# Kernel optimization log

Hardware: AMD Instinct MI355X
Metric: run time of the kernel (lower is better)

## Reference

```python
import jax, jax.numpy as jnp
import numpy as np

STALENESS_LAMBDA = 0.001
TEMPERATURE = 1.0
TOP_K = 3
EPS = 1e-8


def setup_inputs() -> dict:
    key = jax.random.key(0)
    ks = jax.random.split(key, 6)
    B, D, H, E = 131072, 512, 256, 10
    features = jax.random.normal(ks[0], (B, D), dtype=jnp.float32)
    W_proj = jax.random.normal(ks[1], (D, H), dtype=jnp.float32) * 0.02
    b_proj = jnp.zeros((H,), dtype=jnp.float32)
    expert_emb = jax.random.normal(ks[2], (E, H), dtype=jnp.float32) * 0.01
    expert_features = jax.random.normal(ks[3], (E, D), dtype=jnp.float32)
    trust = jax.random.uniform(ks[4], (E,), dtype=jnp.float32)
    delta_t = jax.random.uniform(ks[5], (E,), dtype=jnp.float32) * 100.0
    return {"features": features, "W_proj": W_proj, "b_proj": b_proj,
            "expert_emb": expert_emb, "expert_features": expert_features,
            "trust": trust, "delta_t": delta_t}


def reference(features, W_proj, b_proj, expert_emb, expert_features, trust, delta_t):
    H = W_proj.shape[1]
    # learned gate: sigmoid(proj(x) . e_j / sqrt(H))  -> (B, E)
    proj = features @ W_proj + b_proj                                  # (B, H)
    gate = jax.nn.sigmoid(jnp.einsum('bh,eh->be', proj, expert_emb)
                          / jnp.sqrt(jnp.float32(H)))
    # cosine similarity S_ij mapped to [0, 1]                          # (B, E)
    fn = features / jnp.maximum(jnp.linalg.norm(features, axis=1, keepdims=True), EPS)
    en = expert_features / jnp.maximum(
        jnp.linalg.norm(expert_features, axis=1, keepdims=True), EPS)
    sim = (jnp.einsum('bd,ed->be', fn, en) + 1.0) * 0.5
    # staleness decay e^{-lambda * dt} and base score T*S*decay
    stale = jnp.exp(-STALENESS_LAMBDA * delta_t)                        # (E,)
    score = gate * (trust * stale)[None, :] * sim                       # (B, E)
    probs = jax.nn.softmax(score / TEMPERATURE, axis=-1)                # (B, E)
    topk_w, topk_idx = jax.lax.top_k(probs, TOP_K)                      # (B, K)
    topk_w = topk_w / jnp.sum(topk_w, axis=-1, keepdims=True)
    return topk_w, topk_idx, probs
```

## Files before the change

kernel.cpp:

```cpp
#include <hip/hip_runtime.h>
#include <stdint.h>
#include <math.h>

#define D_DIM 512
#define H_DIM 256
#define E_NUM 10

typedef float f16v __attribute__((ext_vector_type(16)));
typedef float f2 __attribute__((ext_vector_type(2)));

__global__ __launch_bounds__(256) void pre_wg(const float* __restrict__ Wp,
                                              const float* __restrict__ bp,
                                              const float* __restrict__ emb,
                                              float* __restrict__ pk,
                                              float* __restrict__ bg) {
  int gid = blockIdx.x * 256 + threadIdx.x;
  if (gid < E_NUM * D_DIM) {
    int d = gid / E_NUM;
    int e = gid - d * E_NUM;
    const float* wr = Wp + (size_t)d * H_DIM;
    const float* er = emb + (size_t)e * H_DIM;
    float s0 = 0.f, s1 = 0.f, s2 = 0.f, s3 = 0.f;
#pragma unroll 4
    for (int h = 0; h < H_DIM; h += 4) {
      float4 a = *(const float4*)(wr + h);
      float4 b = *(const float4*)(er + h);
      s0 = fmaf(a.x, b.x, s0); s1 = fmaf(a.y, b.y, s1);
      s2 = fmaf(a.z, b.z, s2); s3 = fmaf(a.w, b.w, s3);
    }
    pk[(size_t)d * 20 + e] = ((s0 + s1) + (s2 + s3)) * 0.0625f;
  } else if (gid < E_NUM * D_DIM + E_NUM) {
    int e = gid - E_NUM * D_DIM;
    const float* er = emb + (size_t)e * H_DIM;
    float s = 0.f;
    for (int h = 0; h < H_DIM; ++h) s = fmaf(bp[h], er[h], s);
    bg[e] = s * 0.0625f;
  }
}

__global__ __launch_bounds__(64) void pre_en(const float* __restrict__ ef,
                                             const float* __restrict__ trust,
                                             const float* __restrict__ dtv,
                                             float* __restrict__ pk,
                                             float* __restrict__ cf) {
  int e = blockIdx.x, l = threadIdx.x;
  const float* row = ef + (size_t)e * D_DIM;
  float s = 0.f;
#pragma unroll
  for (int j = 0; j < D_DIM / 64; ++j) { float v = row[l + 64 * j]; s = fmaf(v, v, s); }
#pragma unroll
  for (int o = 32; o; o >>= 1) s += __shfl_xor(s, o, 64);
  float inv = 1.f / fmaxf(sqrtf(s), 1e-8f);
#pragma unroll
  for (int j = 0; j < D_DIM / 64; ++j) {
    int d = l + 64 * j;
    pk[(size_t)d * 20 + 10 + e] = row[d] * inv;
  }
  if (l == 0) cf[e] = trust[e] * expf(-0.001f * dtv[e]);
}

#define WVx(i) ((i) < 16 ? w0[(i) & 15] : (i) < 32 ? w1[(i) & 15] : \
                (i) < 48 ? w2[(i) & 15] : (i) < 64 ? w3[(i) & 15] : w4[(i) & 15])

__global__ __launch_bounds__(256, 5) void router_main(
    const float* __restrict__ feat, const float* __restrict__ pk,
    const float* __restrict__ cf, const float* __restrict__ bg,
    float* __restrict__ out, int B) {
  __shared__ float lds[8192];
  const int t = threadIdx.x;
  const int l = t & 63;
  const int w = __builtin_amdgcn_readfirstlane(t >> 6);
  const size_t r0 = (size_t)blockIdx.x * 64;
  const int wbase = w * 2048;

  const int rpp = l >> 2;
  const int qsw = (l & 3) ^ (rpp & 3) ^ ((rpp >> 2) & 3);
  const float* gsrc = feat + (r0 + rpp) * (size_t)D_DIM + w * 128 + qsw * 4;
  const int csw = ((l & 3) ^ ((l >> 2) & 3)) << 2;

  f2 ag[5], as_[5], n2;
#pragma unroll
  for (int i = 0; i < 5; ++i) { ag[i] = f2{0.f, 0.f}; as_[i] = f2{0.f, 0.f}; }
  n2 = f2{0.f, 0.f};

  auto STAGE = [&](int buf, int c) {
#pragma unroll
    for (int j = 0; j < 4; ++j) {
      __builtin_amdgcn_global_load_lds(
          (const __attribute__((address_space(1))) uint32_t*)(gsrc + (size_t)j * 16 * D_DIM + c * 16),
          (__attribute__((address_space(3))) uint32_t*)&lds[wbase + buf * 1024 + j * 256 + (l << 2)],
          16, 0, 0);
    }
  };

  auto COMPUTE = [&](int buf, int c) {
#pragma unroll
    for (int qq = 0; qq < 4; ++qq) {
      f16v w0, w1, w2, w3, w4;
      const float* wp = pk + (size_t)(w * 128 + c * 16 + qq * 4) * 20;
      asm volatile(
          "s_load_dwordx16 %0, %5, 0x0\n"
          "s_load_dwordx16 %1, %5, 0x40\n"
          "s_load_dwordx16 %2, %5, 0x80\n"
          "s_load_dwordx16 %3, %5, 0xc0\n"
          "s_load_dwordx16 %4, %5, 0x100\n"
          "s_waitcnt lgkmcnt(0)"
          : "=&s"(w0), "=&s"(w1), "=&s"(w2), "=&s"(w3), "=&s"(w4)
          : "s"(wp));
      float4 f = *(const float4*)&lds[wbase + buf * 1024 + l * 16 + ((qq << 2) ^ csw)];
#pragma unroll
      for (int q = 0; q < 4; ++q) {
        const float fq = (q == 0) ? f.x : (q == 1) ? f.y : (q == 2) ? f.z : f.w;
        const f2 fq2 = {fq, fq};
#pragma unroll
        for (int j = 0; j < 5; ++j) {
          const int bgi = q * 20 + 2 * j;
          f2 wg2 = {WVx(bgi), WVx(bgi + 1)};
          ag[j] = __builtin_elementwise_fma(fq2, wg2, ag[j]);
        }
#pragma unroll
        for (int j = 0; j < 5; ++j) {
          const int bsi = q * 20 + 10 + 2 * j;
          f2 ws2 = {WVx(bsi), WVx(bsi + 1)};
          as_[j] = __builtin_elementwise_fma(fq2, ws2, as_[j]);
        }
      }
      f2 p0 = {f.x, f.y}, p1 = {f.z, f.w};
      n2 = __builtin_elementwise_fma(p0, p0, n2);
      n2 = __builtin_elementwise_fma(p1, p1, n2);
    }
  };

  STAGE(0, 0); STAGE(1, 1);
#pragma unroll 1
  for (int c = 0; c < 6; ++c) {
    asm volatile("s_waitcnt vmcnt(4)" ::: "memory");
    __builtin_amdgcn_sched_barrier(0);
    COMPUTE(c & 1, c);
    asm volatile("s_waitcnt lgkmcnt(0)" ::: "memory");
    __builtin_amdgcn_sched_barrier(0);
    STAGE(c & 1, c + 2);
  }
  asm volatile("s_waitcnt vmcnt(4)" ::: "memory");
  __builtin_amdgcn_sched_barrier(0);
  COMPUTE(0, 6);
  asm volatile("s_waitcnt vmcnt(0)" ::: "memory");
  __builtin_amdgcn_sched_barrier(0);
  COMPUTE(1, 7);

  float acc[21];
#pragma unroll
  for (int e = 0; e < E_NUM; ++e) { acc[e] = ag[e >> 1][e & 1]; acc[10 + e] = as_[e >> 1][e & 1]; }
  acc[20] = n2.x + n2.y;

  if (w) {
    float* rp = &lds[wbase + l * 24];
#pragma unroll
    for (int i = 0; i < 21; ++i) rp[i] = acc[i];
  }
  __syncthreads();
  if (w == 0) {
#pragma unroll
    for (int s = 1; s < 4; ++s) {
      const float* rp = &lds[s * 2048 + l * 24];
#pragma unroll
      for (int i = 0; i < 21; ++i) acc[i] += rp[i];
    }

    const float inv = 1.f / fmaxf(sqrtf(acc[20]), 1e-8f);
    float probs[E_NUM];
    float m = -1e30f;
#pragma unroll
    for (int e = 0; e < E_NUM; ++e) {
      float logit = acc[e] + bg[e];
      float gate = 1.f / (1.f + __expf(-logit));
      float sim = fmaf(acc[10 + e] * inv, 0.5f, 0.5f);
      float sc = gate * cf[e] * sim;
      probs[e] = sc;
      m = fmaxf(m, sc);
    }
    float Z = 0.f;
#pragma unroll
    for (int e = 0; e < E_NUM; ++e) { float pe = __expf(probs[e] - m); probs[e] = pe; Z += pe; }
    const float invZ = 1.f / Z;
#pragma unroll
    for (int e = 0; e < E_NUM; ++e) probs[e] *= invZ;

    int i0 = 0; float b0 = probs[0];
#pragma unroll
    for (int e = 1; e < E_NUM; ++e) if (probs[e] > b0) { b0 = probs[e]; i0 = e; }
    int i1 = -1; float b1 = -1.f;
#pragma unroll
    for (int e = 0; e < E_NUM; ++e) if (e != i0 && probs[e] > b1) { b1 = probs[e]; i1 = e; }
    int i2 = -1; float b2 = -1.f;
#pragma unroll
    for (int e = 0; e < E_NUM; ++e) if (e != i0 && e != i1 && probs[e] > b2) { b2 = probs[e]; i2 = e; }

    const float wnorm = 1.f / (b0 + b1 + b2);
    const size_t row = r0 + l;
    float* ow = out + row * 3;
    ow[0] = b0 * wnorm; ow[1] = b1 * wnorm; ow[2] = b2 * wnorm;
    float* oi = out + (size_t)B * 3 + row * 3;
    oi[0] = (float)i0; oi[1] = (float)i1; oi[2] = (float)i2;
    float* op = out + (size_t)B * 6 + row * E_NUM;
#pragma unroll
    for (int e = 0; e < E_NUM; ++e) op[e] = probs[e];
  }
}

extern "C" void kernel_launch(void* const* d_in, const int* in_sizes, int n_in,
                              void* d_out, int out_size, void* d_ws, size_t ws_size,
                              hipStream_t stream) {
  const float* feat  = (const float*)d_in[0];
  const float* Wp    = (const float*)d_in[1];
  const float* bp    = (const float*)d_in[2];
  const float* emb   = (const float*)d_in[3];
  const float* ef    = (const float*)d_in[4];
  const float* trust = (const float*)d_in[5];
  const float* dtv   = (const float*)d_in[6];
  float* out = (float*)d_out;

  float* pk = (float*)d_ws;
  float* cf = pk + D_DIM * 20;
  float* bg = cf + E_NUM;

  const int B = in_sizes[0] / D_DIM;

  hipLaunchKernelGGL(pre_wg, dim3((E_NUM * D_DIM + E_NUM + 255) / 256), dim3(256),
                     0, stream, Wp, bp, emb, pk, bg);
  hipLaunchKernelGGL(pre_en, dim3(E_NUM), dim3(64), 0, stream, ef, trust, dtv, pk, cf);
  hipLaunchKernelGGL(router_main, dim3(B / 64), dim3(256), 0, stream,
                     feat, pk, cf, bg, out, B);
}
```

Baseline: 81.60 us.

## Share a triple-buffered LDS ring across waves with block barriers

```diff
diff --git a/kernel.cpp b/kernel.cpp
--- a/kernel.cpp
+++ b/kernel.cpp
@@ -62,21 +62,19 @@
 #define WVx(i) ((i) < 16 ? w0[(i) & 15] : (i) < 32 ? w1[(i) & 15] : \
                 (i) < 48 ? w2[(i) & 15] : (i) < 64 ? w3[(i) & 15] : w4[(i) & 15])
 
-__global__ __launch_bounds__(256, 5) void router_main(
+__global__ __launch_bounds__(256, 6) void router_main(
     const float* __restrict__ feat, const float* __restrict__ pk,
     const float* __restrict__ cf, const float* __restrict__ bg,
     float* __restrict__ out, int B) {
-  __shared__ float lds[8192];
+  __shared__ float lds[6144];
   const int t = threadIdx.x;
   const int l = t & 63;
   const int w = __builtin_amdgcn_readfirstlane(t >> 6);
   const size_t r0 = (size_t)blockIdx.x * 64;
-  const int wbase = w * 2048;
-
-  const int rpp = l >> 2;
-  const int qsw = (l & 3) ^ (rpp & 3) ^ ((rpp >> 2) & 3);
-  const float* gsrc = feat + (r0 + rpp) * (size_t)D_DIM + w * 128 + qsw * 4;
-  const int csw = ((l & 3) ^ ((l >> 2) & 3)) << 2;
+
+  const float* gsrc = feat + (r0 + w * 16 + (l >> 3)) * (size_t)D_DIM
+                      + (((l & 7) ^ (l >> 3)) << 2);
+  const int dst0 = w * 512 + (l << 2);
 
   f2 ag[5], as_[5], n2;
 #pragma unroll
@@ -85,19 +83,19 @@
 
   auto STAGE = [&](int buf, int c) {
 #pragma unroll
-    for (int j = 0; j < 4; ++j) {
+    for (int j = 0; j < 2; ++j) {
       __builtin_amdgcn_global_load_lds(
-          (const __attribute__((address_space(1))) uint32_t*)(gsrc + (size_t)j * 16 * D_DIM + c * 16),
-          (__attribute__((address_space(3))) uint32_t*)&lds[wbase + buf * 1024 + j * 256 + (l << 2)],
+          (const __attribute__((address_space(1))) uint32_t*)(gsrc + (size_t)j * 8 * D_DIM + c * 32),
+          (__attribute__((address_space(3))) uint32_t*)&lds[buf * 2048 + dst0 + j * 256],
           16, 0, 0);
     }
   };
 
   auto COMPUTE = [&](int buf, int c) {
 #pragma unroll
-    for (int qq = 0; qq < 4; ++qq) {
+    for (int sub = 0; sub < 2; ++sub) {
       f16v w0, w1, w2, w3, w4;
-      const float* wp = pk + (size_t)(w * 128 + c * 16 + qq * 4) * 20;
+      const float* wp = pk + (size_t)(c * 32 + w * 8 + sub * 4) * 20;
       asm volatile(
           "s_load_dwordx16 %0, %5, 0x0\n"
           "s_load_dwordx16 %1, %5, 0x40\n"
@@ -107,7 +105,8 @@
           "s_waitcnt lgkmcnt(0)"
           : "=&s"(w0), "=&s"(w1), "=&s"(w2), "=&s"(w3), "=&s"(w4)
           : "s"(wp));
-      float4 f = *(const float4*)&lds[wbase + buf * 1024 + l * 16 + ((qq << 2) ^ csw)];
+      const int slot = (2 * w + sub) ^ (l & 7);
+      float4 f = *(const float4*)&lds[buf * 2048 + l * 32 + slot * 4];
 #pragma unroll
       for (int q = 0; q < 4; ++q) {
         const float fq = (q == 0) ? f.x : (q == 1) ? f.y : (q == 2) ? f.z : f.w;
@@ -132,21 +131,21 @@
   };
 
   STAGE(0, 0); STAGE(1, 1);
+  int cb = 0, sb = 2;
 #pragma unroll 1
-  for (int c = 0; c < 6; ++c) {
-    asm volatile("s_waitcnt vmcnt(4)" ::: "memory");
+  for (int c = 0; c < 16; ++c) {
+    if (c < 15) asm volatile("s_waitcnt vmcnt(2)" ::: "memory");
+    else        asm volatile("s_waitcnt vmcnt(0)" ::: "memory");
+    __builtin_amdgcn_s_barrier();
     __builtin_amdgcn_sched_barrier(0);
-    COMPUTE(c & 1, c);
+    if (c < 14) STAGE(sb, c + 2);
+    COMPUTE(cb, c);
     asm volatile("s_waitcnt lgkmcnt(0)" ::: "memory");
     __builtin_amdgcn_sched_barrier(0);
-    STAGE(c & 1, c + 2);
-  }
-  asm volatile("s_waitcnt vmcnt(4)" ::: "memory");
-  __builtin_amdgcn_sched_barrier(0);
-  COMPUTE(0, 6);
-  asm volatile("s_waitcnt vmcnt(0)" ::: "memory");
-  __builtin_amdgcn_sched_barrier(0);
-  COMPUTE(1, 7);
+    cb = (cb == 2) ? 0 : cb + 1;
+    sb = (sb == 2) ? 0 : sb + 1;
+  }
+  __syncthreads();
 
   float acc[21];
 #pragma unroll
@@ -154,15 +153,15 @@
   acc[20] = n2.x + n2.y;
 
   if (w) {
-    float* rp = &lds[wbase + l * 24];
+    float* rp = &lds[(w - 1) * 1344 + l * 21];
 #pragma unroll
     for (int i = 0; i < 21; ++i) rp[i] = acc[i];
   }
   __syncthreads();
   if (w == 0) {
 #pragma unroll
-    for (int s = 1; s < 4; ++s) {
-      const float* rp = &lds[s * 2048 + l * 24];
+    for (int s = 0; s < 3; ++s) {
+      const float* rp = &lds[s * 1344 + l * 21];
 #pragma unroll
       for (int i = 0; i < 21; ++i) acc[i] += rp[i];
     }
```

Result: faster. 72.86 us (-10.7%).
